# Optimization experiments

Measured on AMD Instinct MI355X. Metric: run time of the kernel, lower is better.

The kernel has to match this reference:

```python
import jax, jax.numpy as jnp
import numpy as np

NUM_EXPERTS = 64
HIDDEN = 2048
SINKHORN_ITERS = 30
EPS = 1e-08


def setup_inputs() -> dict:
    key = jax.random.key(0)
    k1, k2 = jax.random.split(key)
    hidden_states = jax.random.normal(k1, (4, 2048, HIDDEN), dtype=jnp.float32)
    # torch Linear default init ~ U(-1/sqrt(H), 1/sqrt(H))
    bound = 1.0 / np.sqrt(HIDDEN)
    W = jax.random.uniform(k2, (NUM_EXPERTS, HIDDEN), dtype=jnp.float32,
                           minval=-bound, maxval=bound)
    return {"hidden_states": hidden_states, "W": W}


def _sinkhorn(cost, num_iters=SINKHORN_ITERS):
    # cost: (T, E) float32 logits
    cost = jnp.exp(cost)
    T, E = cost.shape
    d0 = jnp.ones((T,), dtype=cost.dtype)
    d1 = jnp.ones((E,), dtype=cost.dtype)

    def body(i, carry):
        d0, d1 = carry
        d0 = (1.0 / T) / (jnp.sum(d1 * cost, axis=1) + EPS)
        d1 = (1.0 / E) / (jnp.sum(d0[:, None] * cost, axis=0) + EPS)
        return (d0, d1)

    d0, d1 = jax.lax.fori_loop(0, num_iters, body, (d0, d1))
    return d1 * cost * d0[:, None]


def reference(hidden_states, W):
    # router logits: (B, S, H) @ (H, E) -> flatten to (T, E)
    logits = jnp.einsum('bsh,eh->bse', hidden_states, W)
    router_logits = logits.reshape(-1, NUM_EXPERTS)
    # expert affinities (original uses float64 sigmoid; use float32 for jax default)
    expert_affinities = jax.nn.sigmoid(router_logits.astype(jnp.float32))
    expert_affinities = expert_affinities.astype(hidden_states.dtype)
    # Sinkhorn balancing on detached logits (training path)
    sinkroute = _sinkhorn(jax.lax.stop_gradient(router_logits).astype(jnp.float32))
    expert_index = jnp.argmax(sinkroute, axis=1, keepdims=True).astype(jnp.int32)
    return (router_logits, expert_affinities, expert_index)
```

## Files before the change

kernel.cpp:

```cpp
#include <hip/hip_runtime.h>
#include <math.h>

#define T_TOKENS 8192
#define NEXP 64
#define HID 2048
#define NITER 30
#define SINK_BLOCKS 32
#define WREG 131072

typedef __bf16 bf16_t;
typedef bf16_t bf16x8 __attribute__((ext_vector_type(8)));
typedef float  f32x4  __attribute__((ext_vector_type(4)));

__device__ __forceinline__ void gload_lds16(const void* g, void* l) {
    __builtin_amdgcn_global_load_lds(
        (const __attribute__((address_space(1))) unsigned int*)g,
        (__attribute__((address_space(3))) unsigned int*)l, 16, 0, 0);
}

__global__ __launch_bounds__(256)
void prep_whl(const float* __restrict__ W, bf16_t* __restrict__ wsw)
{
    int gid = blockIdx.x * 256 + threadIdx.x;
    int region = gid >> 14;
    int qid = gid & 16383;
    int c = qid >> 9, L = qid & 511;
    int r = L >> 3, slot = L & 7;
    int qi = slot ^ (r & 7);
    const float* src = W + (size_t)r * HID + c * 64 + qi * 8;
    float4 v0 = *(const float4*)src;
    float4 v1 = *(const float4*)(src + 4);
    float x[8] = {v0.x, v0.y, v0.z, v0.w, v1.x, v1.y, v1.z, v1.w};
    bf16x8 q;
#pragma unroll
    for (int i = 0; i < 8; i++) {
        bf16_t h = (bf16_t)x[i];
        q[i] = (region == 0) ? h : (bf16_t)(x[i] - (float)h);
    }
    *(bf16x8*)(wsw + (size_t)region * WREG + (size_t)qid * 8) = q;
}

__global__ __launch_bounds__(256, 2)
void gemm_splitk(const float* __restrict__ A, const bf16_t* __restrict__ Wq,
                 float* __restrict__ part)
{
    __shared__ float  sA[2][32 * 64];
    __shared__ bf16_t sW[2][2][64 * 64];

    const int tid = threadIdx.x, lane = tid & 63, wv = tid >> 6;
    const int ks   = blockIdx.x & 1;
    const int tok0 = (blockIdx.x >> 1) * 32;
    const int mgrp = wv >> 1, ngrp = wv & 1;
    const int g = lane >> 4, m = lane & 15;
    const int arow = mgrp * 16 + m;
    const int m7 = m & 7;

    f32x4 acc0 = {0.f, 0.f, 0.f, 0.f}, acc1 = {0.f, 0.f, 0.f, 0.f};

    int ap[2], acs[2];
#pragma unroll
    for (int j = 0; j < 2; j++) {
        int p = (wv * 2 + j) * 64 + lane;
        ap[j] = p;
        int r = p >> 4, slot = p & 15;
        acs[j] = slot ^ (r & 7);
    }

#define STAGE_CHUNK(cc, dst)                                                    \
    {                                                                           \
        const int _cc = (cc);                                                   \
        _Pragma("unroll")                                                       \
        for (int j = 0; j < 2; j++) {                                           \
            int r = ap[j] >> 4;                                                 \
            const float* src = A + (size_t)(tok0 + r) * HID + ks * 1024         \
                             + _cc * 64 + acs[j] * 4;                           \
            gload_lds16(src, &sA[dst][(wv * 2 + j) * 256]);                     \
        }                                                                       \
        const size_t chb = ((size_t)(ks * 16 + _cc) * 512) * 8;                 \
        _Pragma("unroll")                                                       \
        for (int j = 0; j < 2; j++) {                                           \
            size_t q8 = chb + (size_t)((wv * 2 + j) * 64 + lane) * 8;           \
            gload_lds16(Wq + q8,        &sW[dst][0][(wv * 2 + j) * 512]);       \
            gload_lds16(Wq + WREG + q8, &sW[dst][1][(wv * 2 + j) * 512]);       \
        }                                                                       \
    }

    STAGE_CHUNK(0, 0);
    __syncthreads();

    for (int cc = 0; cc < 16; ++cc) {
        const int buf = cc & 1, nb = buf ^ 1;
        if (cc + 1 < 16) STAGE_CHUNK(cc + 1, nb);

        const float*  sAc = sA[buf];
        const bf16_t* sWh = sW[buf][0];
        const bf16_t* sWl = sW[buf][1];
#pragma unroll
        for (int k32 = 0; k32 < 2; ++k32) {
            int s0 = (k32 * 8 + g * 2) ^ m7;
            float4 x0 = *(const float4*)&sAc[arow * 64 + s0 * 4];
            float4 x1 = *(const float4*)&sAc[arow * 64 + (s0 ^ 1) * 4];
            float xs[8] = {x0.x, x0.y, x0.z, x0.w, x1.x, x1.y, x1.z, x1.w};
            bf16x8 fAh, fAl;
#pragma unroll
            for (int i = 0; i < 8; i++) {
                bf16_t h = (bf16_t)xs[i];
                fAh[i] = h; fAl[i] = (bf16_t)(xs[i] - (float)h);
            }
            const int q = k32 * 4 + g;
            {
                int off = (ngrp * 32 + m) * 64 + (q ^ m7) * 8;
                bf16x8 fWh = *(const bf16x8*)&sWh[off];
                bf16x8 fWl = *(const bf16x8*)&sWl[off];
                acc0 = __builtin_amdgcn_mfma_f32_16x16x32_bf16(fAh, fWh, acc0, 0, 0, 0);
                acc0 = __builtin_amdgcn_mfma_f32_16x16x32_bf16(fAh, fWl, acc0, 0, 0, 0);
                acc0 = __builtin_amdgcn_mfma_f32_16x16x32_bf16(fAl, fWh, acc0, 0, 0, 0);
            }
            {
                int off = (ngrp * 32 + 16 + m) * 64 + (q ^ m7) * 8;
                bf16x8 fWh = *(const bf16x8*)&sWh[off];
                bf16x8 fWl = *(const bf16x8*)&sWl[off];
                acc1 = __builtin_amdgcn_mfma_f32_16x16x32_bf16(fAh, fWh, acc1, 0, 0, 0);
                acc1 = __builtin_amdgcn_mfma_f32_16x16x32_bf16(fAh, fWl, acc1, 0, 0, 0);
                acc1 = __builtin_amdgcn_mfma_f32_16x16x32_bf16(fAl, fWh, acc1, 0, 0, 0);
            }
        }
        __syncthreads();
    }

    float* pb = part + (size_t)ks * T_TOKENS * 64;
#pragma unroll
    for (int i = 0; i < 4; i++) {
        int t = tok0 + mgrp * 16 + g * 4 + i;
        pb[(size_t)t * 64 + ngrp * 32 + m]      = acc0[i];
        pb[(size_t)t * 64 + ngrp * 32 + 16 + m] = acc1[i];
    }
#undef STAGE_CHUNK
}

__global__ __launch_bounds__(256, 1)
void sinkhorn_v4(const float* __restrict__ part,
                 float* __restrict__ out,
                 float* __restrict__ sd,
                 float* __restrict__ fl)
{
    __shared__ float tile[4][64 * 68];
    __shared__ float d1_lds[64];
    __shared__ float pl[4][64];
    const int tid = threadIdx.x, bid = blockIdx.x;
    const int wave = tid >> 6, lane = tid & 63;
    const int t = bid * 256 + tid;

    float* logits = out;
    float* aff    = out + (size_t)T_TOKENS * 64;
    float* idx    = out + (size_t)2 * T_TOKENS * 64;

    const float* p0 = part + (size_t)t * 64;
    const float* p1 = part + (size_t)T_TOKENS * 64 + (size_t)t * 64;

    float c[64];
#pragma unroll
    for (int e4 = 0; e4 < 16; e4++) {
        float4 a = *(const float4*)(p0 + e4 * 4);
        float4 b = *(const float4*)(p1 + e4 * 4);
        float4 v = {a.x + b.x, a.y + b.y, a.z + b.z, a.w + b.w};
        *(float4*)(logits + (size_t)t * 64 + e4 * 4) = v;
        float4 sg;
        sg.x = (v.x >= 0.f) ? 1.f / (1.f + expf(-v.x)) : expf(v.x) / (1.f + expf(v.x));
        sg.y = (v.y >= 0.f) ? 1.f / (1.f + expf(-v.y)) : expf(v.y) / (1.f + expf(v.y));
        sg.z = (v.z >= 0.f) ? 1.f / (1.f + expf(-v.z)) : expf(v.z) / (1.f + expf(v.z));
        sg.w = (v.w >= 0.f) ? 1.f / (1.f + expf(-v.w)) : expf(v.w) / (1.f + expf(v.w));
        *(float4*)(aff + (size_t)t * 64 + e4 * 4) = sg;
        c[e4 * 4 + 0] = expf(v.x);
        c[e4 * 4 + 1] = expf(v.y);
        c[e4 * 4 + 2] = expf(v.z);
        c[e4 * 4 + 3] = expf(v.w);
    }
    if (tid < 64) d1_lds[tid] = 1.0f;
    __syncthreads();

    float d0 = 0.f;
    float* tw = tile[wave];

    for (int iter = 0; iter < NITER; ++iter) {
        float s = 0.f;
#pragma unroll
        for (int e4 = 0; e4 < 16; e4++) {
            float4 dv = *(const float4*)(&d1_lds[e4 * 4]);
            s = fmaf(c[e4 * 4 + 0], dv.x, s);
            s = fmaf(c[e4 * 4 + 1], dv.y, s);
            s = fmaf(c[e4 * 4 + 2], dv.z, s);
            s = fmaf(c[e4 * 4 + 3], dv.w, s);
        }
        d0 = (1.0f / 8192.0f) / (s + 1e-8f);

#pragma unroll
        for (int e4 = 0; e4 < 16; e4++) {
            float4 v;
            v.x = c[e4 * 4 + 0] * d0; v.y = c[e4 * 4 + 1] * d0;
            v.z = c[e4 * 4 + 2] * d0; v.w = c[e4 * 4 + 3] * d0;
            *(float4*)(&tw[lane * 68 + e4 * 4]) = v;
        }
        __syncthreads();
        float colsum = 0.f;
#pragma unroll 16
        for (int j = 0; j < 64; j++) colsum += tw[j * 68 + lane];
        pl[wave][lane] = colsum;
        __syncthreads();

        if (tid < 64) {
            float S = pl[0][tid] + pl[1][tid] + pl[2][tid] + pl[3][tid];
            __hip_atomic_store(&sd[(size_t)(iter * SINK_BLOCKS + bid) * 64 + tid], S,
                               __ATOMIC_RELAXED, __HIP_MEMORY_SCOPE_AGENT);
            if (tid == 0) {
                __builtin_amdgcn_fence(__ATOMIC_RELEASE, "agent");
                __hip_atomic_store(&fl[iter * SINK_BLOCKS + bid], 1.0f,
                                   __ATOMIC_RELAXED, __HIP_MEMORY_SCOPE_AGENT);
            }
            if (tid < SINK_BLOCKS) {
                int guard = 0;
                for (;;) {
                    float f = __hip_atomic_load(&fl[iter * SINK_BLOCKS + tid],
                                                __ATOMIC_RELAXED, __HIP_MEMORY_SCOPE_AGENT);
                    if (f > 0.f || ++guard >= (1 << 20)) break;
                    __builtin_amdgcn_s_sleep(1);
                }
            }
            const float* base = sd + (size_t)iter * SINK_BLOCKS * 64 + tid;
            float v[SINK_BLOCKS];
#pragma unroll
            for (int b = 0; b < SINK_BLOCKS; b++)
                v[b] = __hip_atomic_load(base + b * 64, __ATOMIC_RELAXED,
                                         __HIP_MEMORY_SCOPE_AGENT);
            float S2 = 0.f;
#pragma unroll
            for (int b = 0; b < SINK_BLOCKS; b++) S2 += v[b];
            d1_lds[tid] = (1.0f / 64.0f) / (S2 + 1e-8f);
        }
        __syncthreads();
    }

    float best = -1.0f; int bi = 0;
#pragma unroll
    for (int e4 = 0; e4 < 16; e4++) {
        float4 dv = *(const float4*)(&d1_lds[e4 * 4]);
        float vv0 = (dv.x * c[e4 * 4 + 0]) * d0;
        float vv1 = (dv.y * c[e4 * 4 + 1]) * d0;
        float vv2 = (dv.z * c[e4 * 4 + 2]) * d0;
        float vv3 = (dv.w * c[e4 * 4 + 3]) * d0;
        if (vv0 > best) { best = vv0; bi = e4 * 4 + 0; }
        if (vv1 > best) { best = vv1; bi = e4 * 4 + 1; }
        if (vv2 > best) { best = vv2; bi = e4 * 4 + 2; }
        if (vv3 > best) { best = vv3; bi = e4 * 4 + 3; }
    }
    idx[t] = (float)bi;
}

extern "C" void kernel_launch(void* const* d_in, const int* in_sizes, int n_in,
                              void* d_out, int out_size, void* d_ws, size_t ws_size,
                              hipStream_t stream)
{
    (void)in_sizes; (void)n_in; (void)out_size; (void)ws_size;
    const float* hs = (const float*)d_in[0];
    const float* W  = (const float*)d_in[1];
    float* out      = (float*)d_out;

    bf16_t* wsw = (bf16_t*)d_ws;
    float*  part = (float*)d_ws + 131072;
    float*  sd   = part + 2 * T_TOKENS * 64;
    float*  fl   = sd + NITER * SINK_BLOCKS * 64;

    prep_whl<<<128, 256, 0, stream>>>(W, wsw);
    gemm_splitk<<<512, 256, 0, stream>>>(hs, wsw, part);
    sinkhorn_v4<<<SINK_BLOCKS, 256, 0, stream>>>(part, out, sd, fl);
}
```

Before: 220.3 us.

## Poll Sinkhorn partial sums directly, cache transposed costs in LDS, deepen split-K

The cross-block Sinkhorn exchange no longer uses a separate flag array with a release fence. Each block now spins on the partial-sum values themselves until all of them are positive, which removes one global round trip per iteration. The exp-cost matrix is written transposed into LDS once, so each column sum becomes a dot product with a shared d0 vector instead of rewriting a scaled tile every iteration. The GEMM split-K goes from 2 to 4 segments with more blocks and higher occupancy, at the cost of more partial-sum traffic and relaxed-ordering risk in the value-based readiness check.

```diff
diff --git a/kernel.cpp b/kernel.cpp
--- a/kernel.cpp
+++ b/kernel.cpp
@@ -6,6 +6,7 @@
 #define HID 2048
 #define NITER 30
 #define SINK_BLOCKS 32
+#define KSEG 4
 #define WREG 131072
 
 typedef __bf16 bf16_t;
@@ -40,7 +41,7 @@
     *(bf16x8*)(wsw + (size_t)region * WREG + (size_t)qid * 8) = q;
 }
 
-__global__ __launch_bounds__(256, 2)
+__global__ __launch_bounds__(256, 3)
 void gemm_splitk(const float* __restrict__ A, const bf16_t* __restrict__ Wq,
                  float* __restrict__ part)
 {
@@ -48,8 +49,8 @@
     __shared__ bf16_t sW[2][2][64 * 64];
 
     const int tid = threadIdx.x, lane = tid & 63, wv = tid >> 6;
-    const int ks   = blockIdx.x & 1;
-    const int tok0 = (blockIdx.x >> 1) * 32;
+    const int ks   = blockIdx.x & 3;
+    const int tok0 = (blockIdx.x >> 2) * 32;
     const int mgrp = wv >> 1, ngrp = wv & 1;
     const int g = lane >> 4, m = lane & 15;
     const int arow = mgrp * 16 + m;
@@ -72,11 +73,11 @@
         _Pragma("unroll")                                                       \
         for (int j = 0; j < 2; j++) {                                           \
             int r = ap[j] >> 4;                                                 \
-            const float* src = A + (size_t)(tok0 + r) * HID + ks * 1024         \
+            const float* src = A + (size_t)(tok0 + r) * HID + ks * 512          \
                              + _cc * 64 + acs[j] * 4;                           \
             gload_lds16(src, &sA[dst][(wv * 2 + j) * 256]);                     \
         }                                                                       \
-        const size_t chb = ((size_t)(ks * 16 + _cc) * 512) * 8;                 \
+        const size_t chb = ((size_t)(ks * 8 + _cc) * 512) * 8;                  \
         _Pragma("unroll")                                                       \
         for (int j = 0; j < 2; j++) {                                           \
             size_t q8 = chb + (size_t)((wv * 2 + j) * 64 + lane) * 8;           \
@@ -88,9 +89,9 @@
     STAGE_CHUNK(0, 0);
     __syncthreads();
 
-    for (int cc = 0; cc < 16; ++cc) {
+    for (int cc = 0; cc < 8; ++cc) {
         const int buf = cc & 1, nb = buf ^ 1;
-        if (cc + 1 < 16) STAGE_CHUNK(cc + 1, nb);
+        if (cc + 1 < 8) STAGE_CHUNK(cc + 1, nb);
 
         const float*  sAc = sA[buf];
         const bf16_t* sWh = sW[buf][0];
@@ -139,31 +140,31 @@
 }
 
 __global__ __launch_bounds__(256, 1)
-void sinkhorn_v4(const float* __restrict__ part,
+void sinkhorn_v5(const float* __restrict__ part,
                  float* __restrict__ out,
-                 float* __restrict__ sd,
-                 float* __restrict__ fl)
-{
-    __shared__ float tile[4][64 * 68];
+                 float* __restrict__ sd)
+{
+    __shared__ float tileT[64][260];
+    __shared__ float d0_lds[256];
     __shared__ float d1_lds[64];
     __shared__ float pl[4][64];
     const int tid = threadIdx.x, bid = blockIdx.x;
-    const int wave = tid >> 6, lane = tid & 63;
     const int t = bid * 256 + tid;
 
     float* logits = out;
     float* aff    = out + (size_t)T_TOKENS * 64;
     float* idx    = out + (size_t)2 * T_TOKENS * 64;
 
-    const float* p0 = part + (size_t)t * 64;
-    const float* p1 = part + (size_t)T_TOKENS * 64 + (size_t)t * 64;
-
     float c[64];
 #pragma unroll
     for (int e4 = 0; e4 < 16; e4++) {
-        float4 a = *(const float4*)(p0 + e4 * 4);
-        float4 b = *(const float4*)(p1 + e4 * 4);
-        float4 v = {a.x + b.x, a.y + b.y, a.z + b.z, a.w + b.w};
+        float4 v = *(const float4*)(part + (size_t)t * 64 + e4 * 4);
+#pragma unroll
+        for (int s = 1; s < KSEG; s++) {
+            float4 p = *(const float4*)(part + (size_t)s * T_TOKENS * 64
+                                             + (size_t)t * 64 + e4 * 4);
+            v.x += p.x; v.y += p.y; v.z += p.z; v.w += p.w;
+        }
         *(float4*)(logits + (size_t)t * 64 + e4 * 4) = v;
         float4 sg;
         sg.x = (v.x >= 0.f) ? 1.f / (1.f + expf(-v.x)) : expf(v.x) / (1.f + expf(v.x));
@@ -176,11 +177,13 @@
         c[e4 * 4 + 2] = expf(v.z);
         c[e4 * 4 + 3] = expf(v.w);
     }
+#pragma unroll
+    for (int e = 0; e < 64; e++) tileT[e][tid] = c[e];
     if (tid < 64) d1_lds[tid] = 1.0f;
     __syncthreads();
 
+    const int pe = tid & 63, pq = tid >> 6;
     float d0 = 0.f;
-    float* tw = tile[wave];
 
     for (int iter = 0; iter < NITER; ++iter) {
         float s = 0.f;
@@ -193,45 +196,40 @@
             s = fmaf(c[e4 * 4 + 3], dv.w, s);
         }
         d0 = (1.0f / 8192.0f) / (s + 1e-8f);
-
-#pragma unroll
-        for (int e4 = 0; e4 < 16; e4++) {
-            float4 v;
-            v.x = c[e4 * 4 + 0] * d0; v.y = c[e4 * 4 + 1] * d0;
-            v.z = c[e4 * 4 + 2] * d0; v.w = c[e4 * 4 + 3] * d0;
-            *(float4*)(&tw[lane * 68 + e4 * 4]) = v;
-        }
-        __syncthreads();
-        float colsum = 0.f;
-#pragma unroll 16
-        for (int j = 0; j < 64; j++) colsum += tw[j * 68 + lane];
-        pl[wave][lane] = colsum;
+        d0_lds[tid] = d0;
+        __syncthreads();
+
+        float cs = 0.f;
+        const float* rowp = &tileT[pe][pq * 64];
+        const float* d0p  = &d0_lds[pq * 64];
+#pragma unroll
+        for (int j = 0; j < 16; j++) {
+            float4 cv = *(const float4*)(rowp + j * 4);
+            float4 dv = *(const float4*)(d0p + j * 4);
+            cs = fmaf(cv.x, dv.x, cs);
+            cs = fmaf(cv.y, dv.y, cs);
+            cs = fmaf(cv.z, dv.z, cs);
+            cs = fmaf(cv.w, dv.w, cs);
+        }
+        pl[pq][pe] = cs;
         __syncthreads();
 
         if (tid < 64) {
             float S = pl[0][tid] + pl[1][tid] + pl[2][tid] + pl[3][tid];
             __hip_atomic_store(&sd[(size_t)(iter * SINK_BLOCKS + bid) * 64 + tid], S,
                                __ATOMIC_RELAXED, __HIP_MEMORY_SCOPE_AGENT);
-            if (tid == 0) {
-                __builtin_amdgcn_fence(__ATOMIC_RELEASE, "agent");
-                __hip_atomic_store(&fl[iter * SINK_BLOCKS + bid], 1.0f,
-                                   __ATOMIC_RELAXED, __HIP_MEMORY_SCOPE_AGENT);
-            }
-            if (tid < SINK_BLOCKS) {
-                int guard = 0;
-                for (;;) {
-                    float f = __hip_atomic_load(&fl[iter * SINK_BLOCKS + tid],
-                                                __ATOMIC_RELAXED, __HIP_MEMORY_SCOPE_AGENT);
-                    if (f > 0.f || ++guard >= (1 << 20)) break;
-                    __builtin_amdgcn_s_sleep(1);
-                }
-            }
             const float* base = sd + (size_t)iter * SINK_BLOCKS * 64 + tid;
             float v[SINK_BLOCKS];
-#pragma unroll
-            for (int b = 0; b < SINK_BLOCKS; b++)
-                v[b] = __hip_atomic_load(base + b * 64, __ATOMIC_RELAXED,
-                                         __HIP_MEMORY_SCOPE_AGENT);
+            bool ok = false; int guard = 0;
+            while (!ok && guard++ < (1 << 20)) {
+                ok = true;
+#pragma unroll
+                for (int b = 0; b < SINK_BLOCKS; b++)
+                    v[b] = __hip_atomic_load(base + b * 64, __ATOMIC_RELAXED,
+                                             __HIP_MEMORY_SCOPE_AGENT);
+#pragma unroll
+                for (int b = 0; b < SINK_BLOCKS; b++) ok = ok && (v[b] > 0.f);
+            }
             float S2 = 0.f;
 #pragma unroll
             for (int b = 0; b < SINK_BLOCKS; b++) S2 += v[b];
@@ -265,12 +263,11 @@
     const float* W  = (const float*)d_in[1];
     float* out      = (float*)d_out;
 
-    bf16_t* wsw = (bf16_t*)d_ws;
+    bf16_t* wsw  = (bf16_t*)d_ws;
     float*  part = (float*)d_ws + 131072;
-    float*  sd   = part + 2 * T_TOKENS * 64;
-    float*  fl   = sd + NITER * SINK_BLOCKS * 64;
+    float*  sd   = part + (size_t)KSEG * T_TOKENS * 64;
 
     prep_whl<<<128, 256, 0, stream>>>(W, wsw);
-    gemm_splitk<<<512, 256, 0, stream>>>(hs, wsw, part);
-    sinkhorn_v4<<<SINK_BLOCKS, 256, 0, stream>>>(part, out, sd, fl);
-}
+    gemm_splitk<<<1024, 256, 0, stream>>>(hs, wsw, part);
+    sinkhorn_v5<<<SINK_BLOCKS, 256, 0, stream>>>(part, out, sd);
+}
```

Result: slower. 237.1 us (+7.6%).
